# Performance work log

Hardware: AMD Instinct MI355X
Metric: run time of the kernel (lower is better)

The kernel has to match this reference:

```python
import jax, jax.numpy as jnp
import numpy as np

# ---- static config (mirrors CE defaults) ----
PS = 7        # patch size
WS = 27       # search window (per side)
S0 = 4        # query stride (stride0)
KS = 100      # k_s: top-k kept by search
KA = 100      # k_a: top-k used for aggregation
SCALE = 10.0  # softmax_scale
CI = 16       # inter_channels


def conv2d(x, w, b, pad):
    y = jax.lax.conv_general_dilated(
        x, w, (1, 1), [(pad, pad), (pad, pad)],
        dimension_numbers=("NCHW", "OIHW", "NCHW"))
    return y + b[None, :, None, None]


def all_patches(v):
    """[T,C,H,W] -> [T, H*W, C*PS*PS]; top-left anchored PSxPS patches,
    edge-clamped at the border (dnls-style bounded patch extraction)."""
    t, c, h, w = v.shape
    ii = jnp.clip(jnp.arange(h)[:, None] + jnp.arange(PS)[None, :], 0, h - 1)
    jj = jnp.clip(jnp.arange(w)[:, None] + jnp.arange(PS)[None, :], 0, w - 1)
    p = v[:, :, ii][:, :, :, :, jj]          # [T,C,H,PS,W,PS]
    p = p.transpose(0, 2, 4, 1, 3, 5)        # [T,H,W,C,PS,PS]
    return p.reshape(t, h * w, c * PS * PS)


def setup_inputs():
    key = jax.random.key(0)
    ks = jax.random.split(key, 4)
    vid = jax.random.normal(ks[0], (4, 64, 128, 128), jnp.float32)
    g_w = jax.random.normal(ks[1], (CI, 64, 3, 3), jnp.float32) * 0.05
    g_b = jnp.zeros((CI,), jnp.float32)
    theta_w = jax.random.normal(ks[2], (CI, 64, 1, 1), jnp.float32) * 0.1
    theta_b = jnp.zeros((CI,), jnp.float32)
    return {"vid": vid, "g_w": g_w, "g_b": g_b,
            "theta_w": theta_w, "theta_b": theta_b}


def reference(vid, g_w, g_b, theta_w, theta_b):
    t, c, h, w = vid.shape
    nH, nW = h // S0, w // S0
    Q, N = nH * nW, h * w

    # feature extraction (g -> search features, theta -> aggregation values)
    v1 = conv2d(vid, g_w, g_b, 1)          # [T,CI,H,W]
    v2 = conv2d(vid, theta_w, theta_b, 0)  # [T,CI,H,W]

    # windowed k-NN patch search: query grid (stride0) vs all keys (stride1=1)
    P1 = all_patches(v1)                                    # [T,N,D]
    qis = jnp.arange(nH) * S0
    qjs = jnp.arange(nW) * S0
    qflat = (qis[:, None] * w + qjs[None, :]).reshape(-1)   # [Q]
    Pq = P1[:, qflat]                                       # [T,Q,D]
    scores = jnp.einsum("tqd,tnd->tqn", Pq, P1)             # [T,Q,N]

    off = jnp.arange(WS) - WS // 2
    ci = jnp.clip(qis[:, None] + off, 0, h - 1)             # [nH,WS]
    cj = jnp.clip(qjs[:, None] + off, 0, w - 1)             # [nW,WS]
    cand = (ci[:, None, :, None] * w + cj[None, :, None, :]).reshape(Q, WS * WS)
    dists = jnp.take_along_axis(scores, cand[None], axis=2)  # [T,Q,WS*WS]

    d_k, widx = jax.lax.top_k(dists, KS)                    # [T,Q,KS]
    inds = jnp.take_along_axis(jnp.broadcast_to(cand[None], dists.shape),
                               widx, axis=2)                # flat key positions

    # top-k softmax aggregation weights
    wgt = jax.nn.softmax(d_k[..., :KA] * SCALE, axis=-1)    # [T,Q,KA]
    inds_a = inds[..., :KA]

    # wpsum: weighted sum of value patches gathered at neighbor indices,
    # expressed as sparse-scatter matrix @ dense patch matrix
    A = jnp.zeros((t, Q, N), scores.dtype).at[
        jnp.arange(t)[:, None, None],
        jnp.arange(Q)[None, :, None],
        inds_a].add(wgt)                                    # [T,Q,N]
    P2 = all_patches(v2)                                    # [T,N,D]
    z = jnp.einsum("tqn,tnd->tqd", A, P2)                   # [T,Q,CI*PS*PS]

    # ifold: scatter-add overlapping patches + count normalization
    z = z.reshape(t, Q, CI, PS, PS).transpose(0, 2, 1, 3, 4)
    z = z.reshape(t, CI, Q * PS * PS)
    ri = jnp.clip(qis[:, None] + jnp.arange(PS), 0, h - 1)  # [nH,PS]
    rj = jnp.clip(qjs[:, None] + jnp.arange(PS), 0, w - 1)  # [nW,PS]
    pix = (ri[:, None, :, None] * w + rj[None, :, None, :]).reshape(-1)
    Y = jnp.zeros((t, CI, N), z.dtype).at[:, :, pix].add(z)
    Zc = jnp.zeros((N,), z.dtype).at[pix].add(1.0)
    y = (Y / Zc).reshape(t, CI, h, w)
    return y
```

## Files before the change

### kernel.cpp

```cpp
#include <hip/hip_runtime.h>
#include <hip/hip_bf16.h>

#define T_ 4
#define C_ 64
#define H_ 128
#define W_ 128
#define CI_ 16
#define PS_ 7
#define NC_ 729
#define NCP_ 732
#define S0_ 4
#define KS_ 100
#define NQ_ 1024
#define SCALE_ 10.0f
#define HW_ (H_*W_)
#define RW_ 45
#define LCAP_ 768
#define CB_ 8
#define CH_ 32

typedef float v2f __attribute__((ext_vector_type(2)));
#if __has_builtin(__builtin_elementwise_fma)
#define VFMA(a, b, c) __builtin_elementwise_fma((a), (b), (c))
#else
#define VFMA(a, b, c) ((a) * (b) + (c))
#endif

__device__ __forceinline__ float4 f4add(float4 a, float4 b) {
  return make_float4(a.x + b.x, a.y + b.y, a.z + b.z, a.w + b.w);
}

__device__ __forceinline__ float4 colfix(float4 r, bool loB, bool hiB) {
  float4 o;
  o.x = loB ? 0.f : (hiB ? r.y : r.x);
  o.y = loB ? r.x : (hiB ? r.z : r.y);
  o.z = loB ? r.y : (hiB ? r.w : r.z);
  o.w = loB ? r.z : (hiB ? 0.f : r.w);
  return o;
}

__global__ __launch_bounds__(128, 1) void conv_fused_kernel(
    const float* __restrict__ vid, const float* __restrict__ gw,
    const float* __restrict__ gb, const float* __restrict__ tw,
    const float* __restrict__ tb, float4* __restrict__ v1A,
    float4* __restrict__ v1B, float4* __restrict__ v2A,
    float4* __restrict__ v2B) {
  __shared__ float wls[CH_ * 9 * 4];
  __shared__ float tls[CH_ * 4];
  const int tid = threadIdx.x;
  const int g = blockIdx.y;
  const int t = blockIdx.z & 3, half = blockIdx.z >> 2;
  for (int m = tid; m < CH_ * 9 * 4; m += 128) {
    int co = m & 3, ck = m >> 2;
    wls[m] = gw[((size_t)(g * 4 + co) * C_) * 9 + half * (CH_ * 9) + ck];
  }
  for (int m = tid; m < CH_ * 4; m += 128) {
    int o = m & 3, c = m >> 2;
    tls[m] = tw[(g * 4 + o) * C_ + half * CH_ + c];
  }
  __syncthreads();
  const int ti0 = (blockIdx.x >> 3) * 16, tj0 = (blockIdx.x & 7) * 16;
  const int u = tid >> 3, v = tid & 7;
  const int i = ti0 + u, j0 = tj0 + 2 * v;
  const int c0 = j0 - 1;
  const int c0c = min(max(c0, 0), W_ - 4);
  const bool loB = (c0 < 0), hiB = (c0 > W_ - 4);
  const int rm1 = max(i - 1, 0), rp1 = min(i + 1, H_ - 1);
  const float mk0 = (i > 0) ? 1.f : 0.f;
  const float mk2 = (i < H_ - 1) ? 1.f : 0.f;
  const int o0 = rm1 * W_ + c0c, o1 = i * W_ + c0c, o2 = rp1 * W_ + c0c;

  float accA[4], accB[4], acc1A[4], acc1B[4];
#pragma unroll
  for (int co = 0; co < 4; ++co) {
    float bg = half ? 0.f : gb[g * 4 + co];
    float bt = half ? 0.f : tb[g * 4 + co];
    accA[co] = bg; accB[co] = bg;
    acc1A[co] = bt; acc1B[co] = bt;
  }

  const float* vb = vid + ((size_t)t * C_ + half * CH_) * HW_;
#pragma unroll 1
  for (int cb = 0; cb < CH_; cb += CB_) {
    float4 r[CB_][3];
#pragma unroll
    for (int c = 0; c < CB_; ++c) {
      const float* p = vb + (size_t)(cb + c) * HW_;
      r[c][0] = *(const float4*)(p + o0);
      r[c][1] = *(const float4*)(p + o1);
      r[c][2] = *(const float4*)(p + o2);
    }
#pragma unroll
    for (int c = 0; c < CB_; ++c) {
      float4 f0 = colfix(r[c][0], loB, hiB);
      float4 f1 = colfix(r[c][1], loB, hiB);
      float4 f2 = colfix(r[c][2], loB, hiB);
      f0.x *= mk0; f0.y *= mk0; f0.z *= mk0; f0.w *= mk0;
      f2.x *= mk2; f2.y *= mk2; f2.z *= mk2; f2.w *= mk2;
      const float* wc = &wls[(cb + c) * 36];
      const float* tc = &tls[(cb + c) * 4];
      float e0[4] = {f0.x, f0.y, f0.z, f0.w};
      float e1[4] = {f1.x, f1.y, f1.z, f1.w};
      float e2[4] = {f2.x, f2.y, f2.z, f2.w};
#pragma unroll
      for (int co = 0; co < 4; ++co) {
        acc1A[co] = fmaf(tc[co], e1[1], acc1A[co]);
        acc1B[co] = fmaf(tc[co], e1[2], acc1B[co]);
      }
#pragma unroll
      for (int kj = 0; kj < 3; ++kj) {
#pragma unroll
        for (int co = 0; co < 4; ++co) {
          accA[co] = fmaf(wc[(0 * 3 + kj) * 4 + co], e0[kj],     accA[co]);
          accB[co] = fmaf(wc[(0 * 3 + kj) * 4 + co], e0[kj + 1], accB[co]);
          accA[co] = fmaf(wc[(1 * 3 + kj) * 4 + co], e1[kj],     accA[co]);
          accB[co] = fmaf(wc[(1 * 3 + kj) * 4 + co], e1[kj + 1], accB[co]);
          accA[co] = fmaf(wc[(2 * 3 + kj) * 4 + co], e2[kj],     accA[co]);
          accB[co] = fmaf(wc[(2 * 3 + kj) * 4 + co], e2[kj + 1], accB[co]);
        }
      }
    }
  }
  float4* v1o = half ? v1B : v1A;
  float4* v2o = half ? v2B : v2A;
  const size_t o = ((size_t)g * T_ + t) * HW_ + i * W_ + j0;
  v1o[o]     = make_float4(accA[0], accA[1], accA[2], accA[3]);
  v1o[o + 1] = make_float4(accB[0], accB[1], accB[2], accB[3]);
  v2o[o]     = make_float4(acc1A[0], acc1A[1], acc1A[2], acc1A[3]);
  v2o[o + 1] = make_float4(acc1B[0], acc1B[1], acc1B[2], acc1B[3]);
}

__global__ __launch_bounds__(512, 2) void dist_kernel(
    const float4* __restrict__ v1A, const float4* __restrict__ v1B,
    float* __restrict__ out, int cbase, int nch) {
  __shared__ float4 Rs[2][2048];
  const int tid = threadIdx.x;
  const int t = blockIdx.y;
  const int qi0 = (blockIdx.x >> 3) * 16, qj0 = (blockIdx.x & 7) * 16;
  const int w = tid >> 6, lane = tid & 63;
  const int pr = w >> 2, dj = (w & 3) * 4;
  const int rbase = 8 * pr;
  const int qi_p = qi0 + rbase;
  const int qj = qj0 + dj;
  const int la = lane >> 1, bg = lane & 1;
  const int b_lo = max(13 - qj, 0);
  const int bs = bg ? 13 : b_lo;
  const int a_lo0 = max(13 - qi_p, 0);
  const int a_lo1 = max(9 - qi_p, 0);
  const bool compute_ok = (la < 31);

  int soff[4];
#pragma unroll
  for (int k = 0; k < 4; ++k) {
    int p = min(tid + 512 * k, RW_ * RW_ - 1);
    int uu = p / RW_, vv = p - uu * RW_;
    int row = min(max(qi0 - 13 + uu, 0), H_ - 1);
    int col = min(max(qj0 - 13 + vv, 0), W_ - 1);
    soff[k] = row * W_ + col;
  }

  v2f acc0[14], acc1[14];
#pragma unroll
  for (int j = 0; j < 14; ++j) { acc0[j] = (v2f){0.f, 0.f}; acc1[j] = (v2f){0.f, 0.f}; }

  float4 st[4];
  {
    const float4* sA = v1A + ((size_t)cbase * T_ + t) * HW_;
    const float4* sB = v1B + ((size_t)cbase * T_ + t) * HW_;
#pragma unroll
    for (int k = 0; k < 4; ++k) st[k] = f4add(sA[soff[k]], sB[soff[k]]);
  }
  int cur = 0;
#pragma unroll 1
  for (int ci = 0; ci < nch; ++ci) {
    float4* buf = &Rs[cur][0];
#pragma unroll
    for (int k = 0; k < 4; ++k) buf[tid + 512 * k] = st[k];
    if (ci + 1 < nch) {
      const float4* sA = v1A + ((size_t)(cbase + ci + 1) * T_ + t) * HW_;
      const float4* sB = v1B + ((size_t)(cbase + ci + 1) * T_ + t) * HW_;
#pragma unroll
      for (int k = 0; k < 4; ++k) st[k] = f4add(sA[soff[k]], sB[soff[k]]);
    }
    __syncthreads();
    if (compute_ok) {
#pragma unroll 1
      for (int r = 0; r < 7; ++r) {
        v2f q0lo[7], q0hi[7], q1lo[7], q1hi[7];
        const float4* q0row = &buf[(rbase + 13 + r) * RW_ + dj + 13];
#pragma unroll
        for (int s = 0; s < 7; ++s) {
          float4 qq = q0row[s];
          q0lo[s] = (v2f){qq.x, qq.y};
          q0hi[s] = (v2f){qq.z, qq.w};
          float4 q2 = q0row[4 * RW_ + s];
          q1lo[s] = (v2f){q2.x, q2.y};
          q1hi[s] = (v2f){q2.z, q2.w};
        }
        const float4* crow = &buf[(rbase + la + r) * RW_ + dj + bs];
#pragma unroll
        for (int y = 0; y < 20; ++y) {
          float4 vv4 = crow[y];
          v2f vlo = (v2f){vv4.x, vv4.y}, vhi = (v2f){vv4.z, vv4.w};
          const int s_lo = (y > 13) ? (y - 13) : 0;
          const int s_hi = (y < 6) ? y : 6;
#pragma unroll
          for (int s = s_lo; s <= s_hi; ++s) {
            int j = y - s;
            acc0[j] = VFMA(q0lo[s], vlo, acc0[j]);
            acc0[j] = VFMA(q0hi[s], vhi, acc0[j]);
            acc1[j] = VFMA(q1lo[s], vlo, acc1[j]);
            acc1[j] = VFMA(q1hi[s], vhi, acc1[j]);
          }
        }
      }
    }
    cur ^= 1;
  }
  if (compute_ok) {
    const int q0q = ((qi_p >> 2) << 5) + (qj >> 2);
    if (la >= a_lo0 && la <= 26) {
      float* o = out + ((size_t)t * NQ_ + q0q) * NCP_ + la * 27 + bs;
#pragma unroll
      for (int j = 0; j < 14; ++j) o[j] = acc0[j].x + acc0[j].y;
    }
    const int a1 = la - 4;
    if (a1 >= a_lo1 && a1 <= 26) {
      float* o = out + ((size_t)t * NQ_ + (q0q + 32)) * NCP_ + a1 * 27 + bs;
#pragma unroll
      for (int j = 0; j < 14; ++j) o[j] = acc1[j].x + acc1[j].y;
    }
  }
}

__global__ __launch_bounds__(256) void select_kernel(
    const float* __restrict__ distA, const float* __restrict__ distB, int dual,
    int* __restrict__ sel_n, float* __restrict__ sel_w,
    float* __restrict__ wsum_out) {
  __shared__ float dist[NC_];
  __shared__ unsigned int ukey[NC_];
  __shared__ float redf[4];
  __shared__ unsigned int hist[256];
  __shared__ int lk[LCAP_];
  __shared__ unsigned int lkey[LCAP_];
  __shared__ unsigned int scal[6];

  const int tid = threadIdx.x;
  const int lane = tid & 63, wid = tid >> 6;
  const int q = blockIdx.x, t = blockIdx.y;
  const int qi = (q >> 5) * S0_, qj = (q & 31) * S0_;
  const int a_lo = max(13 - qi, 0), b_lo = max(13 - qj, 0);
  const size_t base = ((size_t)t * NQ_ + q) * NCP_;

  for (int h = tid; h < 256; h += 256) hist[h] = 0;
  if (tid == 0) { scal[2] = 0; scal[3] = 0; }
  float lmax = -INFINITY;
  if (a_lo == 0 && b_lo == 0) {
    if (tid < 182) {
      float4 d4 = *(const float4*)(distA + base + 4 * tid);
      if (dual) {
        float4 b4 = *(const float4*)(distB + base + 4 * tid);
        d4.x += b4.x; d4.y += b4.y; d4.z += b4.z; d4.w += b4.w;
      }
      float dv[4] = {d4.x, d4.y, d4.z, d4.w};
#pragma unroll
      for (int e = 0; e < 4; ++e) {
        int k = 4 * tid + e;
        float d = dv[e];
        dist[k] = d;
        unsigned int u = __float_as_uint(d);
        ukey[k] = u ^ (((unsigned int)((int)u >> 31)) | 0x80000000u);
        lmax = fmaxf(lmax, d);
      }
    } else if (tid == 182) {
      float d = distA[base + 728];
      if (dual) d += distB[base + 728];
      dist[728] = d;
      unsigned int u = __float_as_uint(d);
      ukey[728] = u ^ (((unsigned int)((int)u >> 31)) | 0x80000000u);
      lmax = d;
    }
  } else {
    for (int k = tid; k < NC_; k += 256) {
      int aa = k / 27, bb = k - aa * 27;
      int kk = max(aa, a_lo) * 27 + max(bb, b_lo);
      float d = distA[base + kk];
      if (dual) d += distB[base + kk];
      dist[k] = d;
      unsigned int u = __float_as_uint(d);
      ukey[k] = u ^ (((unsigned int)((int)u >> 31)) | 0x80000000u);
      lmax = fmaxf(lmax, d);
    }
  }
#pragma unroll
  for (int off = 32; off > 0; off >>= 1)
    lmax = fmaxf(lmax, __shfl_down(lmax, off, 64));
  if (lane == 0) redf[wid] = lmax;
  __syncthreads();
  const float dmax = fmaxf(fmaxf(redf[0], redf[1]), fmaxf(redf[2], redf[3]));
  for (int k = tid; k < NC_; k += 256) atomicAdd(&hist[ukey[k] >> 24], 1u);
  __syncthreads();
  if (wid == 0) {
    int s4 = (int)(hist[lane * 4] + hist[lane * 4 + 1] + hist[lane * 4 + 2] + hist[lane * 4 + 3]);
    int s = s4;
#pragma unroll
    for (int off = 1; off < 64; off <<= 1) {
      int o = __shfl_down(s, off, 64);
      if (lane + off < 64) s += o;
    }
    int above = s - s4;
    if (above < KS_ && s >= KS_) {
      int run = above;
#pragma unroll
      for (int bb = 3; bb >= 0; --bb) {
        int h = (int)hist[lane * 4 + bb];
        if (run + h >= KS_) { scal[0] = (unsigned int)(lane * 4 + bb); scal[1] = (unsigned int)run; break; }
        run += h;
      }
    }
  }
  __syncthreads();
  const unsigned int beta = scal[0];
  const int run = (int)scal[1];
  for (int h = tid; h < 256; h += 256) hist[h] = 0;
  __syncthreads();
  for (int k = tid; k < NC_; k += 256)
    if ((ukey[k] >> 24) == beta) atomicAdd(&hist[(ukey[k] >> 16) & 0xFFu], 1u);
  __syncthreads();
  if (wid == 0) {
    int s4 = (int)(hist[lane * 4] + hist[lane * 4 + 1] + hist[lane * 4 + 2] + hist[lane * 4 + 3]);
    int s = s4;
#pragma unroll
    for (int off = 1; off < 64; off <<= 1) {
      int o = __shfl_down(s, off, 64);
      if (lane + off < 64) s += o;
    }
    int above = run + s - s4;
    if (above < KS_ && run + s >= KS_) {
      int r2 = above;
#pragma unroll
      for (int bb = 3; bb >= 0; --bb) {
        int h = (int)hist[lane * 4 + bb];
        if (r2 + h >= KS_) { scal[4] = (unsigned int)(lane * 4 + bb); scal[5] = (unsigned int)r2; break; }
        r2 += h;
      }
    }
  }
  __syncthreads();
  const unsigned int beta2 = scal[4];
  const int run2 = (int)scal[5];
  const size_t outb = ((size_t)t * NQ_ + q) * KS_;
  float lsum = 0.f;
  for (int k = tid; k < NC_; k += 256) {
    unsigned int key = ukey[k];
    unsigned int bin = key >> 24;
    bool sel = false, bdry = false;
    if (bin > beta) sel = true;
    else if (bin == beta) {
      unsigned int b2 = (key >> 16) & 0xFFu;
      if (b2 > beta2) sel = true;
      else if (b2 == beta2) bdry = true;
    }
    if (sel) {
      unsigned int slot = atomicAdd(&scal[2], 1u);
      int aa = k / 27, bb = k - aa * 27;
      int ni = min(max(qi + aa - 13, 0), H_ - 1);
      int nj = min(max(qj + bb - 13, 0), W_ - 1);
      float wv = __expf(SCALE_ * (dist[k] - dmax));
      sel_n[outb + slot] = (ni << 7) | nj;
      sel_w[outb + slot] = wv;
      lsum += wv;
    } else if (bdry) {
      unsigned int pos = atomicAdd(&scal[3], 1u);
      if (pos < LCAP_) { lk[pos] = k; lkey[pos] = key; }
    }
  }
  __syncthreads();
  const int L = min((int)scal[3], LCAP_);
  for (int i = tid; i < L; i += 256) {
    unsigned int key = lkey[i];
    int k = lk[i];
    int cnt = run2;
    for (int m = 0; m < L; ++m)
      cnt += (int)((lkey[m] > key) || (lkey[m] == key && lk[m] < k));
    if (cnt < KS_) {
      unsigned int slot = atomicAdd(&scal[2], 1u);
      int aa = k / 27, bb = k - aa * 27;
      int ni = min(max(qi + aa - 13, 0), H_ - 1);
      int nj = min(max(qj + bb - 13, 0), W_ - 1);
      float wv = __expf(SCALE_ * (dist[k] - dmax));
      sel_n[outb + slot] = (ni << 7) | nj;
      sel_w[outb + slot] = wv;
      lsum += wv;
    }
  }
#pragma unroll
  for (int off = 32; off > 0; off >>= 1) lsum += __shfl_down(lsum, off, 64);
  __syncthreads();
  if (lane == 0) redf[wid] = lsum;
  __syncthreads();
  if (tid == 0) wsum_out[t * NQ_ + q] = (redf[0] + redf[1]) + (redf[2] + redf[3]);
}

__device__ __forceinline__ int cov_axis(int x) {
  int c = 0;
#pragma unroll
  for (int r = 0; r < 7; ++r) {
    if (x < H_ - 1) {
      int qb = x - r;
      c += (qb >= 0 && (qb & 3) == 0) ? 1 : 0;
    } else {
      c += (r >= 3) ? 1 : 0;
    }
  }
  return c;
}

__global__ __launch_bounds__(1024) void agg_kernel(
    const float4* __restrict__ v2A, const float4* __restrict__ v2B,
    const int* __restrict__ sel_n, const float* __restrict__ sel_w,
    const float* __restrict__ wsum, float* __restrict__ Y) {
  __shared__ float4 Rs[RW_ * RW_];
  __shared__ int s_off[16][KS_];
  __shared__ float s_w[16][KS_];
  const int tid = threadIdx.x;
  const int t = blockIdx.y;
  const int cc0 = blockIdx.z * 2;
  const int qi0 = (blockIdx.x >> 3) * 16, qj0 = (blockIdx.x & 7) * 16;
  const int w = tid >> 6, lane = tid & 63;
  const int di = (w >> 2) * 4, dj = (w & 3) * 4;
  const int qi = qi0 + di, qj = qj0 + dj;
  const int q = ((qi >> 2) << 5) + (qj >> 2);
  const size_t base = ((size_t)t * NQ_ + q) * KS_;
  const float inv = 1.0f / wsum[t * NQ_ + q];
  for (int k = lane; k < KS_; k += 64) {
    int n = sel_n[base + k];
    int ni = n >> 7, nj = n & 127;
    s_off[w][k] = (ni - qi0 + 13) * RW_ + (nj - qj0 + 13);
    s_w[w][k] = sel_w[base + k] * inv;
  }
  const int r = lane / 7, s = lane - r * 7;
  const int myo = r * RW_ + s;
  const int oi = min(qi + r, H_ - 1), oj = min(qj + s, W_ - 1);
  const float invZ = 1.0f / (float)(cov_axis(oi) * cov_axis(oj));
#pragma unroll 1
  for (int ci = 0; ci < 2; ++ci) {
    const int cc = cc0 + ci;
    __syncthreads();
    const float4* sA = v2A + ((size_t)cc * T_ + t) * HW_;
    const float4* sB = v2B + ((size_t)cc * T_ + t) * HW_;
    for (int p = tid; p < RW_ * RW_; p += 1024) {
      int uu = p / RW_, vv = p - uu * RW_;
      int row = min(max(qi0 - 13 + uu, 0), H_ - 1);
      int col = min(max(qj0 - 13 + vv, 0), W_ - 1);
      const int so = row * W_ + col;
      Rs[p] = f4add(sA[so], sB[so]);
    }
    __syncthreads();
    if (lane < 49) {
      float4 acc = make_float4(0.f, 0.f, 0.f, 0.f);
#pragma unroll 4
      for (int k = 0; k < KS_; ++k) {
        float wv = s_w[w][k];
        float4 v = Rs[s_off[w][k] + myo];
        acc.x = fmaf(wv, v.x, acc.x);
        acc.y = fmaf(wv, v.y, acc.y);
        acc.z = fmaf(wv, v.z, acc.z);
        acc.w = fmaf(wv, v.w, acc.w);
      }
      float* yb = Y + (((size_t)t * CI_ + cc * 4) * H_ + oi) * W_ + oj;
      atomicAdd(yb, acc.x * invZ);
      atomicAdd(yb + HW_, acc.y * invZ);
      atomicAdd(yb + 2 * HW_, acc.z * invZ);
      atomicAdd(yb + 3 * HW_, acc.w * invZ);
    }
  }
}

extern "C" void kernel_launch(void* const* d_in, const int* in_sizes, int n_in,
                              void* d_out, int out_size, void* d_ws, size_t ws_size,
                              hipStream_t stream) {
  const float* vid     = (const float*)d_in[0];
  const float* g_w     = (const float*)d_in[1];
  const float* g_b     = (const float*)d_in[2];
  const float* theta_w = (const float*)d_in[3];
  const float* theta_b = (const float*)d_in[4];
  float* Y = (float*)d_out;

  const size_t VSZ = (size_t)4 * T_ * HW_ * 4;
  float* v1A   = (float*)d_ws;
  float* v1B   = v1A + VSZ;
  float* v2A   = v1B + VSZ;
  float* v2B   = v2A + VSZ;
  float* distG = v2B + VSZ;
  int*   sel_n = (int*)(distG + (size_t)T_ * NQ_ * NCP_);
  float* sel_w = (float*)(sel_n + (size_t)T_ * NQ_ * KS_);
  float* wsumv = sel_w + (size_t)T_ * NQ_ * KS_;
  float* distB = wsumv + (size_t)T_ * NQ_;

  const size_t need_dual =
      (VSZ * 4 + (size_t)T_ * NQ_ * NCP_ * 2 +
       (size_t)T_ * NQ_ * KS_ * 2 + (size_t)T_ * NQ_) * sizeof(float);
  const int dual = (ws_size >= need_dual) ? 1 : 0;

  hipMemsetAsync(Y, 0, (size_t)out_size * sizeof(float), stream);

  conv_fused_kernel<<<dim3(64, 4, 2 * T_), 128, 0, stream>>>(
      vid, g_w, g_b, theta_w, theta_b,
      (float4*)v1A, (float4*)v1B, (float4*)v2A, (float4*)v2B);
  if (dual) {
    dist_kernel<<<dim3(64, T_), 512, 0, stream>>>(
        (const float4*)v1A, (const float4*)v1B, distG, 0, 2);
    dist_kernel<<<dim3(64, T_), 512, 0, stream>>>(
        (const float4*)v1A, (const float4*)v1B, distB, 2, 2);
  } else {
    dist_kernel<<<dim3(64, T_), 512, 0, stream>>>(
        (const float4*)v1A, (const float4*)v1B, distG, 0, 4);
  }
  select_kernel<<<dim3(NQ_, T_), 256, 0, stream>>>(distG, distB, dual, sel_n, sel_w, wsumv);
  agg_kernel<<<dim3(64, T_, 2), 1024, 0, stream>>>(
      (const float4*)v2A, (const float4*)v2B, sel_n, sel_w, wsumv, Y);
}
```

Baseline: 250.0 us.

## Merge dual dist launches into one grid and single-buffer shared tile

The two channel-half dist_kernel launches become one launch with blockIdx.z picking the channel half and output buffer, so 512 blocks run concurrently instead of two sequential 256-block launches. The shared-memory tile drops from double to single buffering, with an extra barrier after compute and the next-channel prefetch held in registers. This is meant to raise GPU occupancy and remove one launch and its tail, at the cost of one more __syncthreads per channel iteration.

New measurement: 251.8 us. About the same (+0.7%).

```diff
diff --git a/kernel.cpp b/kernel.cpp
--- a/kernel.cpp
+++ b/kernel.cpp
@@ -132,10 +132,13 @@
 
 __global__ __launch_bounds__(512, 2) void dist_kernel(
     const float4* __restrict__ v1A, const float4* __restrict__ v1B,
-    float* __restrict__ out, int cbase, int nch) {
-  __shared__ float4 Rs[2][2048];
+    float* __restrict__ outG, float* __restrict__ outB, int nch) {
+  __shared__ float4 Rs[2048];
   const int tid = threadIdx.x;
   const int t = blockIdx.y;
+  const int half = blockIdx.z;
+  const int cbase = half * nch;
+  float* out = half ? outB : outG;
   const int qi0 = (blockIdx.x >> 3) * 16, qj0 = (blockIdx.x & 7) * 16;
   const int w = tid >> 6, lane = tid & 63;
   const int pr = w >> 2, dj = (w & 3) * 4;
@@ -170,24 +173,23 @@
 #pragma unroll
     for (int k = 0; k < 4; ++k) st[k] = f4add(sA[soff[k]], sB[soff[k]]);
   }
-  int cur = 0;
 #pragma unroll 1
   for (int ci = 0; ci < nch; ++ci) {
-    float4* buf = &Rs[cur][0];
-#pragma unroll
-    for (int k = 0; k < 4; ++k) buf[tid + 512 * k] = st[k];
+#pragma unroll
+    for (int k = 0; k < 4; ++k) Rs[tid + 512 * k] = st[k];
+    float4 nx[4];
     if (ci + 1 < nch) {
       const float4* sA = v1A + ((size_t)(cbase + ci + 1) * T_ + t) * HW_;
       const float4* sB = v1B + ((size_t)(cbase + ci + 1) * T_ + t) * HW_;
 #pragma unroll
-      for (int k = 0; k < 4; ++k) st[k] = f4add(sA[soff[k]], sB[soff[k]]);
+      for (int k = 0; k < 4; ++k) nx[k] = f4add(sA[soff[k]], sB[soff[k]]);
     }
     __syncthreads();
     if (compute_ok) {
 #pragma unroll 1
       for (int r = 0; r < 7; ++r) {
         v2f q0lo[7], q0hi[7], q1lo[7], q1hi[7];
-        const float4* q0row = &buf[(rbase + 13 + r) * RW_ + dj + 13];
+        const float4* q0row = &Rs[(rbase + 13 + r) * RW_ + dj + 13];
 #pragma unroll
         for (int s = 0; s < 7; ++s) {
           float4 qq = q0row[s];
@@ -197,7 +199,7 @@
           q1lo[s] = (v2f){q2.x, q2.y};
           q1hi[s] = (v2f){q2.z, q2.w};
         }
-        const float4* crow = &buf[(rbase + la + r) * RW_ + dj + bs];
+        const float4* crow = &Rs[(rbase + la + r) * RW_ + dj + bs];
 #pragma unroll
         for (int y = 0; y < 20; ++y) {
           float4 vv4 = crow[y];
@@ -215,7 +217,9 @@
         }
       }
     }
-    cur ^= 1;
+    __syncthreads();
+#pragma unroll
+    for (int k = 0; k < 4; ++k) st[k] = nx[k];
   }
   if (compute_ok) {
     const int q0q = ((qi_p >> 2) << 5) + (qj >> 2);
@@ -509,13 +513,11 @@
       vid, g_w, g_b, theta_w, theta_b,
       (float4*)v1A, (float4*)v1B, (float4*)v2A, (float4*)v2B);
   if (dual) {
-    dist_kernel<<<dim3(64, T_), 512, 0, stream>>>(
-        (const float4*)v1A, (const float4*)v1B, distG, 0, 2);
-    dist_kernel<<<dim3(64, T_), 512, 0, stream>>>(
-        (const float4*)v1A, (const float4*)v1B, distB, 2, 2);
+    dist_kernel<<<dim3(64, T_, 2), 512, 0, stream>>>(
+        (const float4*)v1A, (const float4*)v1B, distG, distB, 2);
   } else {
-    dist_kernel<<<dim3(64, T_), 512, 0, stream>>>(
-        (const float4*)v1A, (const float4*)v1B, distG, 0, 4);
+    dist_kernel<<<dim3(64, T_, 1), 512, 0, stream>>>(
+        (const float4*)v1A, (const float4*)v1B, distG, distB, 4);
   }
   select_kernel<<<dim3(NQ_, T_), 256, 0, stream>>>(distG, distB, dual, sel_n, sel_w, wsumv);
   agg_kernel<<<dim3(64, T_, 2), 1024, 0, stream>>>(
```
